# Kernel optimization log

Measured on AMD Instinct MI355X. Metric: run time of the kernel, lower is better.

## Reference

```python
import jax, jax.numpy as jnp
import numpy as np

N = 100000          # total nodes
E = 3200000         # total edges (avg degree 32)
B = 100             # num graphs
NPG = N // B        # nodes per graph (uniform -> to_dense_batch is a reshape)
D_IN, D_H, D_E, N_CLS = 128, 64, 32, 10


def setup_inputs() -> dict:
    key = jax.random.key(0)
    ks = jax.random.split(key, 12)
    x = jax.random.normal(ks[0], (N, D_IN), jnp.float32)
    # edges strictly within each graph: offset by graph block
    epg = E // B
    offs = (jnp.arange(E, dtype=jnp.int32) // epg) * NPG
    src = jax.random.randint(ks[1], (E,), 0, NPG, jnp.int32) + offs
    dst = jax.random.randint(ks[2], (E,), 0, NPG, jnp.int32) + offs
    edge_index = jnp.stack([src, dst])
    batch = jnp.repeat(jnp.arange(B, dtype=jnp.int32), NPG)

    def glorot(k, fi, fo):
        return jax.random.normal(k, (fi, fo), jnp.float32) * (1.0 / np.sqrt(fi))

    return {
        "x": x, "edge_index": edge_index, "batch": batch,
        "W_a1": glorot(ks[3], D_IN, D_H), "b_a1": jnp.zeros((D_H,), jnp.float32),
        "W_a2": glorot(ks[4], D_H, D_E),  "b_a2": jnp.zeros((D_E,), jnp.float32),
        "W_x1": glorot(ks[5], D_IN, D_H), "b_x1": jnp.zeros((D_H,), jnp.float32),
        "W_x2": glorot(ks[6], D_H, D_E),  "b_x2": jnp.zeros((D_E,), jnp.float32),
        "W_lin": glorot(ks[7], D_E * D_E, N_CLS),
        "b_lin": jnp.zeros((N_CLS,), jnp.float32),
    }


def _gcn(x, W, b, src, dst, n):
    """PyG GCNConv(improved=True): sym-norm with self-loop weight 2."""
    h = x @ W                                                   # [n, out]
    deg = jax.ops.segment_sum(jnp.ones_like(dst, h.dtype), dst, n) + 2.0
    dinv = jax.lax.rsqrt(deg)                                   # [n]
    coef = dinv[src] * dinv[dst]                                # [E]
    agg = jax.ops.segment_sum(h[src] * coef[:, None], dst, n)   # gather-scatter
    agg = agg + (2.0 * dinv * dinv)[:, None] * h                # self-loop term
    return agg + b


def _segment_softmax(v, seg, nseg):
    m = jax.ops.segment_max(v, seg, nseg)
    e = jnp.exp(v - m[seg])
    s = jax.ops.segment_sum(e, seg, nseg)
    return e / s[seg]


def reference(x, edge_index, batch, W_a1, b_a1, W_a2, b_a2,
              W_x1, b_x1, W_x2, b_x2, W_lin, b_lin):
    src, dst = edge_index[0], edge_index[1]
    n = x.shape[0]
    a1 = jax.nn.relu(_gcn(x, W_a1, b_a1, src, dst, n))
    a2 = _segment_softmax(_gcn(a1, W_a2, b_a2, src, dst, n), batch, B)
    x1 = jax.nn.relu(_gcn(x, W_x1, b_x1, src, dst, n))
    x2 = jax.nn.relu(_gcn(x1, W_x2, b_x2, src, dst, n))
    # uniform graph sizes -> to_dense_batch is a reshape (no padding needed)
    a_b = a2.reshape(B, NPG, D_E)
    x_b = x2.reshape(B, NPG, D_E)
    prods = jnp.einsum('bne,bnf->bef', a_b, x_b)   # bmm(a^T, x): [B, D_E, D_E]
    flat = prods.reshape(B, D_E * D_E)
    return jax.nn.softmax(flat @ W_lin + b_lin, axis=-1)
```

## Files before the change

kernel.cpp:

```cpp
#include <hip/hip_runtime.h>
#include <hip/hip_bf16.h>
#include <hip/hip_fp16.h>

#define N_NODES 100000
#define N_EDGES 3200000
#define NB      100
#define NPG     1000
#define EPG     32000
#define DIN     128
#define DH      64
#define DE      32
#define NCLS    10
#define SORT_BLOCKS 104


typedef _Float16 h2_t __attribute__((ext_vector_type(2)));
typedef _Float16 h8_t __attribute__((ext_vector_type(8)));
typedef float    f4_t __attribute__((ext_vector_type(4)));

__device__ __forceinline__ float dot2f(unsigned a, unsigned b, float c) {
#if __has_builtin(__builtin_amdgcn_fdot2)
    return __builtin_amdgcn_fdot2(__builtin_bit_cast(h2_t, a),
                                  __builtin_bit_cast(h2_t, b), c, false);
#else
    float d;
    asm("v_dot2_f32_f16 %0, %1, %2, %3" : "=v"(d) : "v"(a), "v"(b), "v"(c));
    return d;
#endif
}

#define DOT8(rA, rB, dv)                                                        \
    acc[0] = dot2f(__builtin_amdgcn_perm(rB.x, rA.x, 0x05040100u), dv, acc[0]); \
    acc[1] = dot2f(__builtin_amdgcn_perm(rB.x, rA.x, 0x07060302u), dv, acc[1]); \
    acc[2] = dot2f(__builtin_amdgcn_perm(rB.y, rA.y, 0x05040100u), dv, acc[2]); \
    acc[3] = dot2f(__builtin_amdgcn_perm(rB.y, rA.y, 0x07060302u), dv, acc[3]); \
    acc[4] = dot2f(__builtin_amdgcn_perm(rB.z, rA.z, 0x05040100u), dv, acc[4]); \
    acc[5] = dot2f(__builtin_amdgcn_perm(rB.z, rA.z, 0x07060302u), dv, acc[5]); \
    acc[6] = dot2f(__builtin_amdgcn_perm(rB.w, rA.w, 0x05040100u), dv, acc[6]); \
    acc[7] = dot2f(__builtin_amdgcn_perm(rB.w, rA.w, 0x07060302u), dv, acc[7]);


union SharedU {
    struct {
        __align__(16) unsigned short buf[EPG];
        int cnt[NPG];
        int pre[NPG];
        int sm[1024];
        unsigned short dh[NPG];
    } so;
    struct {
        __align__(16) unsigned short wt[128 * 128];
    } w1;
};

__global__ __launch_bounds__(1024) void k_sg(const int* __restrict__ src,
                                             const int* __restrict__ dst,
                                             const float* __restrict__ x,
                                             const float* __restrict__ Wa,
                                             const float* __restrict__ Wx,
                                             int* __restrict__ rowptr,
                                             float* __restrict__ dinv,
                                             unsigned int* __restrict__ esrc,
                                             unsigned short* __restrict__ h16) {
    __shared__ SharedU S;
    int t = threadIdx.x;
    if (blockIdx.x < SORT_BLOCKS) {
        int g = (blockIdx.x & 7) + 8 * (blockIdx.x >> 3);
        if (g >= NB) return;
        int ebase = g * EPG, nbase = g * NPG;
        if (t < NPG) S.so.cnt[t] = 0;
        __syncthreads();
        for (int i = t; i < EPG; i += 1024)
            atomicAdd(&S.so.cnt[dst[ebase + i] - nbase], 1);
        __syncthreads();
        int v = (t < NPG) ? S.so.cnt[t] : 0;
        if (t < NPG) {
            float dv = rsqrtf((float)v + 2.0f);
            dinv[nbase + t] = dv;
            S.so.dh[t] = __half_as_ushort(__float2half_rn(dv));
        }
        S.so.sm[t] = v;
        __syncthreads();
        for (int off = 1; off < 1024; off <<= 1) {
            int xx = (t >= off) ? S.so.sm[t - off] : 0;
            __syncthreads();
            S.so.sm[t] += xx;
            __syncthreads();
        }
        if (t < NPG) {
            int ex = S.so.sm[t] - v;
            S.so.pre[t] = ex;
            rowptr[nbase + t] = ebase + ex;
        }
        if (g == NB - 1 && t == 0) rowptr[N_NODES] = N_EDGES;
        __syncthreads();
        for (int i = t; i < EPG; i += 1024) {
            int e = ebase + i;
            int d = dst[e] - nbase;
            int s = src[e] - nbase;
            int pos = atomicAdd(&S.so.pre[d], 1);
            S.so.buf[pos] = (unsigned short)s;
        }
        __syncthreads();
        uint4* gout = (uint4*)(esrc + ebase);
        const ushort4* lbuf = (const ushort4*)S.so.buf;
        for (int i = t; i < EPG / 4; i += 1024) {
            ushort4 s4 = lbuf[i];
            uint4 o;
            o.x = ((unsigned)s4.x * 16) | ((unsigned)S.so.dh[s4.x] << 16);
            o.y = ((unsigned)s4.y * 16) | ((unsigned)S.so.dh[s4.y] << 16);
            o.z = ((unsigned)s4.z * 16) | ((unsigned)S.so.dh[s4.z] << 16);
            o.w = ((unsigned)s4.w * 16) | ((unsigned)S.so.dh[s4.w] << 16);
            gout[i] = o;
        }
    } else {
        int b = blockIdx.x - SORT_BLOCKS;
        int xcd = b & 7, slot = b >> 3;
        int g = xcd + 8 * (slot >> 2);
        int chunk = slot & 3;
        if (g >= NB) return;
        int row0 = g * NPG + chunk * 250;
        for (int j = 0; j < 4; j++) {
            int idx = t + 1024 * j;
            int k = idx >> 5, c = (idx & 31) * 4;
            float4 v;
            if (c < 64) v = *(const float4*)&Wa[k * 64 + c];
            else        v = *(const float4*)&Wx[k * 64 + (c - 64)];
            float vv[4] = {v.x, v.y, v.z, v.w};
            #pragma unroll
            for (int m = 0; m < 4; m++) {
                int cc = c + m;
                int byte = cc * 256 + ((k * 2) ^ ((cc & 7) << 4));
                *(__half*)((char*)S.w1.wt + byte) = __float2half_rn(vv[m]);
            }
        }
        __syncthreads();
        int w = t >> 6, l = t & 63;
        int lr = l & 15, kq = l >> 4;
        int rowA = row0 + w * 16 + lr;
        int rA = rowA < N_NODES ? rowA : N_NODES - 1;
        const float* xr = &x[(size_t)rA * 128];
        h8_t a[4];
        #pragma unroll
        for (int kc = 0; kc < 4; kc++) {
            float4 lo = *(const float4*)&xr[kc * 32 + kq * 8];
            float4 hi = *(const float4*)&xr[kc * 32 + kq * 8 + 4];
            h8_t av;
            av[0] = (_Float16)lo.x; av[1] = (_Float16)lo.y;
            av[2] = (_Float16)lo.z; av[3] = (_Float16)lo.w;
            av[4] = (_Float16)hi.x; av[5] = (_Float16)hi.y;
            av[6] = (_Float16)hi.z; av[7] = (_Float16)hi.w;
            a[kc] = av;
        }
        f4_t acc[8] = {};
        #pragma unroll
        for (int kc = 0; kc < 4; kc++) {
            #pragma unroll
            for (int n = 0; n < 8; n++) {
                int cc = n * 16 + lr;
                int byte = cc * 256 + (((kc * 32 + kq * 8) * 2) ^ ((cc & 7) << 4));
                h8_t bf = *(h8_t*)((char*)S.w1.wt + byte);
                acc[n] = __builtin_amdgcn_mfma_f32_16x16x32_f16(a[kc], bf, acc[n], 0, 0, 0);
            }
        }
        int rowD = row0 + w * 16 + kq * 4;
        #pragma unroll
        for (int n = 0; n < 8; n++) {
            #pragma unroll
            for (int j = 0; j < 4; j++) {
                int r = rowD + j;
                if (r < N_NODES)
                    h16[(size_t)r * 128 + n * 16 + lr] =
                        __half_as_ushort(__float2half_rn(acc[n][j]));
            }
        }
    }
}


__global__ __launch_bounds__(256) void k_agg128(const unsigned short* __restrict__ h16,
                                                const int* __restrict__ rowptr,
                                                const unsigned int* __restrict__ esrc,
                                                const float* __restrict__ dinv,
                                                const float* __restrict__ ba,
                                                const float* __restrict__ bx,
                                                unsigned short* __restrict__ outB16) {
    int xcd = blockIdx.x & 7, slot = blockIdx.x >> 3;
    int gi = slot / 250, chunk = slot - gi * 250;
    int g = xcd + 8 * gi;
    if (g >= NB) return;
    int nl   = chunk * 4 + (threadIdx.x >> 6);
    int wid  = g * NPG + nl;
    int lane = threadIdx.x & 63;
    int sub = lane >> 4;
    int cl  = lane & 15;
    const uint4* hg4 = (const uint4*)(h16 + g * NPG * 128);
    float acc[8] = {};
    union U8 { uint4 u; __half h[8]; };
    int e0 = rowptr[wid], e1 = rowptr[wid + 1];
    int e = e0;
    for (; e + 16 <= e1; e += 16) {
        unsigned pv0 = esrc[e + sub];
        unsigned pv1 = esrc[e + 4 + sub];
        unsigned pv2 = esrc[e + 8 + sub];
        unsigned pv3 = esrc[e + 12 + sub];
        uint4 r0 = hg4[(pv0 & 0xffffu) + cl];
        uint4 r1 = hg4[(pv1 & 0xffffu) + cl];
        uint4 r2 = hg4[(pv2 & 0xffffu) + cl];
        uint4 r3 = hg4[(pv3 & 0xffffu) + cl];
        unsigned dA = __builtin_amdgcn_perm(pv1, pv0, 0x07060302u);
        unsigned dB = __builtin_amdgcn_perm(pv3, pv2, 0x07060302u);
        DOT8(r0, r1, dA);
        DOT8(r2, r3, dB);
    }
    for (; e + 8 <= e1; e += 8) {
        unsigned pv0 = esrc[e + sub];
        unsigned pv1 = esrc[e + 4 + sub];
        uint4 r0 = hg4[(pv0 & 0xffffu) + cl];
        uint4 r1 = hg4[(pv1 & 0xffffu) + cl];
        unsigned dA = __builtin_amdgcn_perm(pv1, pv0, 0x07060302u);
        DOT8(r0, r1, dA);
    }
    for (; e < e1; e += 4) {
        int ee = e + sub;
        unsigned pv; float scale;
        if (ee < e1) { pv = esrc[ee]; scale = 1.0f; }
        else         { pv = esrc[e];  scale = 0.0f; }
        U8 r; r.u = hg4[(pv & 0xffffu) + cl];
        float dv = scale * __half2float(__ushort_as_half((unsigned short)(pv >> 16)));
        #pragma unroll
        for (int k = 0; k < 8; k++)
            acc[k] += dv * __half2float(r.h[k]);
    }
    #pragma unroll
    for (int k = 0; k < 8; k++) {
        acc[k] += __shfl_xor(acc[k], 16);
        acc[k] += __shfl_xor(acc[k], 32);
    }
    if (sub == 0) {
        float di = dinv[wid];
        float sw = 2.0f * di * di;
        U8 hv; hv.u = hg4[nl * 16 + cl];
        int cl8 = cl * 8;
        const float* bb = (cl8 < 64) ? &ba[cl8] : &bx[cl8 - 64];
        union { __half2 h[4]; uint4 q; } pk;
        #pragma unroll
        for (int k = 0; k < 4; k++) {
            float ox = fmaxf(di * acc[2 * k]     + sw * __half2float(hv.h[2 * k])     + bb[2 * k],     0.0f);
            float oy = fmaxf(di * acc[2 * k + 1] + sw * __half2float(hv.h[2 * k + 1]) + bb[2 * k + 1], 0.0f);
            pk.h[k] = __floats2half2_rn(ox, oy);
        }
        *(uint4*)&outB16[wid * 128 + cl8] = pk.q;
    }
}


__global__ __launch_bounds__(256) void k_agg64(const unsigned short* __restrict__ g16,
                                               const int* __restrict__ rowptr,
                                               const unsigned int* __restrict__ esrc,
                                               const float* __restrict__ dinv,
                                               const float* __restrict__ ba2,
                                               const float* __restrict__ bx2,
                                               float* __restrict__ s2) {
    int xcd = blockIdx.x & 7, slot = blockIdx.x >> 3;
    int gi = slot / 250, chunk = slot - gi * 250;
    int g = xcd + 8 * gi;
    if (g >= NB) return;
    int nl   = chunk * 4 + (threadIdx.x >> 6);
    int wid  = g * NPG + nl;
    int lane = threadIdx.x & 63;
    int sub = lane >> 3;
    int cl  = lane & 7;
    const uint4* gg4 = (const uint4*)(g16 + g * NPG * 64);
    float acc[8] = {};
    union U8 { uint4 u; __half h[8]; };
    int e0 = rowptr[wid], e1 = rowptr[wid + 1];
    int e = e0;
    for (; e + 16 <= e1; e += 16) {
        unsigned pv0 = esrc[e + sub];
        unsigned pv1 = esrc[e + 8 + sub];
        uint4 r0 = gg4[((pv0 & 0xffffu) >> 1) + cl];
        uint4 r1 = gg4[((pv1 & 0xffffu) >> 1) + cl];
        unsigned dA = __builtin_amdgcn_perm(pv1, pv0, 0x07060302u);
        DOT8(r0, r1, dA);
    }
    for (; e < e1; e += 8) {
        int ee = e + sub;
        unsigned pv; float scale;
        if (ee < e1) { pv = esrc[ee]; scale = 1.0f; }
        else         { pv = esrc[e];  scale = 0.0f; }
        U8 r; r.u = gg4[((pv & 0xffffu) >> 1) + cl];
        float dv = scale * __half2float(__ushort_as_half((unsigned short)(pv >> 16)));
        #pragma unroll
        for (int k = 0; k < 8; k++)
            acc[k] += dv * __half2float(r.h[k]);
    }
    #pragma unroll
    for (int k = 0; k < 8; k++) {
        acc[k] += __shfl_xor(acc[k], 8);
        acc[k] += __shfl_xor(acc[k], 16);
        acc[k] += __shfl_xor(acc[k], 32);
    }
    if (sub == 0) {
        float di = dinv[wid];
        float sw = 2.0f * di * di;
        U8 hv; hv.u = gg4[nl * 8 + cl];
        int cl8 = cl * 8;
        float o[8];
        #pragma unroll
        for (int k = 0; k < 8; k++)
            o[k] = di * acc[k] + sw * __half2float(hv.h[k]);
        if (cl8 < 32) {
            #pragma unroll
            for (int k = 0; k < 8; k++) o[k] += ba2[cl8 + k];
        } else {
            #pragma unroll
            for (int k = 0; k < 8; k++) o[k] = fmaxf(o[k] + bx2[cl8 - 32 + k], 0.0f);
        }
        *(float4*)&s2[wid * 64 + cl8]     = make_float4(o[0], o[1], o[2], o[3]);
        *(float4*)&s2[wid * 64 + cl8 + 4] = make_float4(o[4], o[5], o[6], o[7]);
    }
}


__global__ __launch_bounds__(256) void k_gemm2(const unsigned short* __restrict__ Bm16,
                                               const float* __restrict__ Wa2,
                                               const float* __restrict__ Wx2,
                                               unsigned short* __restrict__ g16) {
    __shared__ float xs[64][132];
    __shared__ float ws[64][68];
    int xcd = blockIdx.x & 7, slot = blockIdx.x >> 3;
    int g = xcd + 8 * (slot >> 4);
    int chunk = slot & 15;
    if (g >= NB) return;
    int row0 = g * NPG + chunk * 64;
    int t = threadIdx.x;
    for (int i = 0; i < 4; i++) {
        int idx = t + 256 * i;
        int k = idx >> 4, c4 = idx & 15, c = c4 * 4;
        float4 v;
        if (c < 32) v = *(const float4*)&Wa2[k * 32 + c];
        else        v = *(const float4*)&Wx2[k * 32 + (c - 32)];
        *(float4*)&ws[k][c] = v;
    }
    for (int i = 0; i < 4; i++) {
        int idx = t + 256 * i;
        int r = idx >> 4, c8 = idx & 15;
        int rr = row0 + r; if (rr >= N_NODES) rr = N_NODES - 1;
        union { uint4 u; __half2 h[4]; } pk;
        pk.u = *(const uint4*)&Bm16[rr * 128 + c8 * 8];
        float2 f0 = __half22float2(pk.h[0]);
        float2 f1 = __half22float2(pk.h[1]);
        float2 f2 = __half22float2(pk.h[2]);
        float2 f3 = __half22float2(pk.h[3]);
        int cb = c8 * 8;
        *(float4*)&xs[r][cb]     = make_float4(f0.x, f0.y, f1.x, f1.y);
        *(float4*)&xs[r][cb + 4] = make_float4(f2.x, f2.y, f3.x, f3.y);
    }
    __syncthreads();
    int cg = t & 15, rg = t >> 4;
    int koff = (cg < 8) ? 0 : 64;
    float acc[4][4] = {};
    for (int k = 0; k < 64; k++) {
        float4 w = *(float4*)&ws[k][cg * 4];
        float xv[4];
        for (int i = 0; i < 4; i++) xv[i] = xs[rg * 4 + i][koff + k];
        for (int i = 0; i < 4; i++) {
            acc[i][0] += xv[i] * w.x; acc[i][1] += xv[i] * w.y;
            acc[i][2] += xv[i] * w.z; acc[i][3] += xv[i] * w.w;
        }
    }
    for (int i = 0; i < 4; i++) {
        int r = row0 + rg * 4 + i;
        if (r < N_NODES) {
            union { ushort4 u; __half2 h[2]; } pk;
            pk.h[0] = __floats2half2_rn(acc[i][0], acc[i][1]);
            pk.h[1] = __floats2half2_rn(acc[i][2], acc[i][3]);
            *(ushort4*)&g16[r * 64 + cg * 4] = pk.u;
        }
    }
}


__global__ __launch_bounds__(512) void k_smax(const float* __restrict__ s2,
                                              float* __restrict__ gmax,
                                              float* __restrict__ sinv) {
    __shared__ float red[16][32];
    int g = (blockIdx.x & 7) + 8 * (blockIdx.x >> 3);
    if (g >= NB) return;
    int t = threadIdx.x;
    int c = t & 31, sub = t >> 5;
    size_t base = (size_t)g * NPG;
    float m = -1e30f;
    for (int n = sub; n < NPG; n += 16)
        m = fmaxf(m, s2[(base + n) * 64 + c]);
    red[sub][c] = m; __syncthreads();
    if (sub == 0) {
        for (int j = 1; j < 16; j++) m = fmaxf(m, red[j][c]);
        red[0][c] = m;
        gmax[g * 32 + c] = m;
    }
    __syncthreads();
    m = red[0][c];
    __syncthreads();
    float sum = 0.0f;
    for (int n = sub; n < NPG; n += 16)
        sum += __expf(s2[(base + n) * 64 + c] - m);
    red[sub][c] = sum; __syncthreads();
    if (sub == 0) {
        for (int j = 1; j < 16; j++) sum += red[j][c];
        sinv[g * 32 + c] = 1.0f / sum;
    }
}


__global__ __launch_bounds__(256) void k_pool(const float* __restrict__ s2,
                                              const float* __restrict__ gmax,
                                              float* __restrict__ prods) {
    __shared__ float ta[25][32];
    __shared__ float tx[25][32];
    __shared__ float gm[32];
    int xcd = blockIdx.x & 7, slot = blockIdx.x >> 3;
    int g = xcd + 8 * (slot >> 3);
    int ch = slot & 7;
    if (g >= NB) return;
    int t = threadIdx.x;
    if (t < 32) gm[t] = gmax[g * 32 + t];
    int e  = t >> 3;
    int f4 = t & 7;
    float a0 = 0.f, a1 = 0.f, a2 = 0.f, a3 = 0.f;
    int base = g * NPG + ch * 125;
    for (int n0 = 0; n0 < 125; n0 += 25) {
        __syncthreads();
        for (int i = t; i < 25 * 16; i += 256) {
            int r = i >> 4, c4 = i & 15;
            float4 v = *(const float4*)&s2[(size_t)(base + n0 + r) * 64 + c4 * 4];
            if (c4 < 8) {
                int cb = c4 * 4;
                v.x = __expf(v.x - gm[cb + 0]);
                v.y = __expf(v.y - gm[cb + 1]);
                v.z = __expf(v.z - gm[cb + 2]);
                v.w = __expf(v.w - gm[cb + 3]);
                *(float4*)&ta[r][cb] = v;
            } else {
                *(float4*)&tx[r][(c4 - 8) * 4] = v;
            }
        }
        __syncthreads();
        #pragma unroll 5
        for (int n = 0; n < 25; n++) {
            float a   = ta[n][e];
            float4 xv = *(float4*)&tx[n][f4 * 4];
            a0 += a * xv.x; a1 += a * xv.y; a2 += a * xv.z; a3 += a * xv.w;
        }
    }
    *(float4*)&prods[((size_t)(g * 8 + ch)) * 1024 + e * 32 + f4 * 4] =
        make_float4(a0, a1, a2, a3);
}


__global__ __launch_bounds__(256) void k_head(const float* __restrict__ prods,
                                              const float* __restrict__ sinv,
                                              const float* __restrict__ Wlin,
                                              const float* __restrict__ blin,
                                              float* __restrict__ out) {
    __shared__ float red[4][NCLS];
    int g = (blockIdx.x & 7) + 8 * (blockIdx.x >> 3);
    if (g >= NB) return;
    int t = threadIdx.x;
    float p[NCLS];
    for (int c = 0; c < NCLS; c++) p[c] = 0.0f;
    const float* pg = &prods[(size_t)g * 8 * 1024];
    for (int j = 0; j < 4; j++) {
        int k = t * 4 + j;
        int e = k >> 5;
        float v = 0.0f;
        #pragma unroll
        for (int q = 0; q < 8; q++) v += pg[q * 1024 + k];
        v *= sinv[g * 32 + e];
        const float* wrow = &Wlin[k * NCLS];
        for (int c = 0; c < NCLS; c++) p[c] += v * wrow[c];
    }
    for (int off = 32; off > 0; off >>= 1)
        for (int c = 0; c < NCLS; c++) p[c] += __shfl_down(p[c], off, 64);
    int wave = t >> 6, lane = t & 63;
    if (lane == 0)
        for (int c = 0; c < NCLS; c++) red[wave][c] = p[c];
    __syncthreads();
    if (t == 0) {
        float logits[NCLS]; float mx = -1e30f;
        for (int c = 0; c < NCLS; c++) {
            logits[c] = red[0][c] + red[1][c] + red[2][c] + red[3][c] + blin[c];
            mx = fmaxf(mx, logits[c]);
        }
        float s = 0.0f;
        for (int c = 0; c < NCLS; c++) { logits[c] = expf(logits[c] - mx); s += logits[c]; }
        float inv = 1.0f / s;
        for (int c = 0; c < NCLS; c++) out[g * NCLS + c] = logits[c] * inv;
    }
}


extern "C" void kernel_launch(void* const* d_in, const int* in_sizes, int n_in,
                              void* d_out, int out_size, void* d_ws, size_t ws_size,
                              hipStream_t stream) {
    const float* x    = (const float*)d_in[0];
    const int*   ei   = (const int*)d_in[1];
    const float* Wa1  = (const float*)d_in[3];
    const float* ba1  = (const float*)d_in[4];
    const float* Wa2  = (const float*)d_in[5];
    const float* ba2  = (const float*)d_in[6];
    const float* Wx1  = (const float*)d_in[7];
    const float* bx1  = (const float*)d_in[8];
    const float* Wx2  = (const float*)d_in[9];
    const float* bx2  = (const float*)d_in[10];
    const float* Wlin = (const float*)d_in[11];
    const float* blin = (const float*)d_in[12];
    float* out = (float*)d_out;

    char* w = (char*)d_ws;
    auto alloc = [&](size_t bytes) -> void* {
        void* p = (void*)w;
        w += (bytes + 255) & ~(size_t)255;
        return p;
    };
    int*            rowptr = (int*)alloc((N_NODES + 1) * sizeof(int));
    float*          dinv   = (float*)alloc(N_NODES * sizeof(float));
    unsigned int*   esrc   = (unsigned int*)alloc((size_t)N_EDGES * sizeof(unsigned int));
    float*          gmax   = (float*)alloc(NB * DE * sizeof(float));
    float*          sinv   = (float*)alloc(NB * DE * sizeof(float));
    float*          prods  = (float*)alloc((size_t)NB * 8 * 1024 * sizeof(float));
    unsigned short* h16    = (unsigned short*)alloc((size_t)N_NODES * 128 * sizeof(unsigned short));
    unsigned short* b16    = (unsigned short*)alloc((size_t)N_NODES * 128 * sizeof(unsigned short));
    unsigned short* g16    = (unsigned short*)alloc((size_t)N_NODES * 64 * sizeof(unsigned short));
    float*          s2     = (float*)alloc((size_t)N_NODES * 64 * sizeof(float));

    const int* srcp = ei;
    const int* dstp = ei + N_EDGES;

    k_sg<<<SORT_BLOCKS + 8 * 13 * 4, 1024, 0, stream>>>(srcp, dstp, x, Wa1, Wx1,
                                                        rowptr, dinv, esrc, h16);
    k_agg128<<<8 * 13 * 250, 256, 0, stream>>>(h16, rowptr, esrc, dinv, ba1, bx1, b16);
    k_gemm2<<<8 * 13 * 16, 256, 0, stream>>>(b16, Wa2, Wx2, g16);
    k_agg64<<<8 * 13 * 250, 256, 0, stream>>>(g16, rowptr, esrc, dinv, ba2, bx2, s2);
    k_smax<<<8 * 13, 512, 0, stream>>>(s2, gmax, sinv);
    k_pool<<<8 * 13 * 8, 256, 0, stream>>>(s2, gmax, prods);
    k_head<<<8 * 13, 256, 0, stream>>>(prods, sinv, Wlin, blin, out);
}
```

Before: 311.2 us.

## Split per-graph CSR build into parallel count, scan and global-atomic scatter kernels

Replaces the one-block-per-graph CSR sort, which did counting, scan and scatter in shared memory, with three kernels. Each graph's edges are split across 8 sub-blocks for counting, a scan kernel combines the partial counts into rowptr, cursor and fp16 dinv, and the scatter uses global atomics on cursor across 832 blocks. The aim is to spread the sort over far more blocks than 100 graphs allow. The cost is two extra launches, global atomic traffic, and edge order within each row that is no longer deterministic. The W staging into shared memory is also rewritten to pack four halves per store.

```diff
diff --git a/kernel.cpp b/kernel.cpp
--- a/kernel.cpp
+++ b/kernel.cpp
@@ -11,7 +11,7 @@
 #define DH      64
 #define DE      32
 #define NCLS    10
-#define SORT_BLOCKS 104
+#define SCAT_BLOCKS 832
 
 
 typedef _Float16 h2_t __attribute__((ext_vector_type(2)));
@@ -40,98 +40,104 @@
     acc[7] = dot2f(__builtin_amdgcn_perm(rB.w, rA.w, 0x07060302u), dv, acc[7]);
 
 
-union SharedU {
-    struct {
-        __align__(16) unsigned short buf[EPG];
-        int cnt[NPG];
-        int pre[NPG];
-        int sm[1024];
-        unsigned short dh[NPG];
-    } so;
-    struct {
-        __align__(16) unsigned short wt[128 * 128];
-    } w1;
-};
+__global__ __launch_bounds__(256) void k_cnt(const int* __restrict__ dst,
+                                             int* __restrict__ cnt8) {
+    __shared__ int cnt[NPG];
+    int slice = blockIdx.x >> 3;
+    int g = (blockIdx.x & 7) + 8 * (slice % 13);
+    int sub = slice / 13;
+    if (g >= NB) return;
+    int t = threadIdx.x;
+    for (int i = t; i < NPG; i += 256) cnt[i] = 0;
+    __syncthreads();
+    int ebase = g * EPG + sub * 4000, nbase = g * NPG;
+    for (int i = t; i < 4000; i += 256)
+        atomicAdd(&cnt[dst[ebase + i] - nbase], 1);
+    __syncthreads();
+    for (int i = t; i < NPG; i += 256)
+        cnt8[sub * N_NODES + nbase + i] = cnt[i];
+}
+
+
+__global__ __launch_bounds__(1024) void k_scan(const int* __restrict__ cnt8,
+                                               int* __restrict__ rowptr,
+                                               int* __restrict__ cursor,
+                                               float* __restrict__ dinv,
+                                               unsigned short* __restrict__ dh16) {
+    __shared__ int sm[1024];
+    int g = (blockIdx.x & 7) + 8 * (blockIdx.x >> 3);
+    if (g >= NB) return;
+    int t = threadIdx.x;
+    int nbase = g * NPG, ebase = g * EPG;
+    int v = 0;
+    if (t < NPG) {
+        #pragma unroll
+        for (int s8 = 0; s8 < 8; s8++) v += cnt8[s8 * N_NODES + nbase + t];
+        float dv = rsqrtf((float)v + 2.0f);
+        dinv[nbase + t] = dv;
+        dh16[nbase + t] = __half_as_ushort(__float2half_rn(dv));
+    }
+    sm[t] = v;
+    __syncthreads();
+    for (int off = 1; off < 1024; off <<= 1) {
+        int xx = (t >= off) ? sm[t - off] : 0;
+        __syncthreads();
+        sm[t] += xx;
+        __syncthreads();
+    }
+    if (t < NPG) {
+        int ex = ebase + sm[t] - v;
+        rowptr[nbase + t] = ex;
+        cursor[nbase + t] = ex;
+    }
+    if (g == NB - 1 && t == 0) rowptr[N_NODES] = N_EDGES;
+}
+
 
 __global__ __launch_bounds__(1024) void k_sg(const int* __restrict__ src,
                                              const int* __restrict__ dst,
                                              const float* __restrict__ x,
                                              const float* __restrict__ Wa,
                                              const float* __restrict__ Wx,
-                                             int* __restrict__ rowptr,
-                                             float* __restrict__ dinv,
+                                             int* __restrict__ cursor,
+                                             const unsigned short* __restrict__ dh16,
                                              unsigned int* __restrict__ esrc,
                                              unsigned short* __restrict__ h16) {
-    __shared__ SharedU S;
-    int t = threadIdx.x;
-    if (blockIdx.x < SORT_BLOCKS) {
-        int g = (blockIdx.x & 7) + 8 * (blockIdx.x >> 3);
+    __shared__ __align__(16) unsigned short wt[16384];
+    int t = threadIdx.x;
+    if (blockIdx.x < SCAT_BLOCKS) {
+        int slice = blockIdx.x >> 3;
+        int g = (blockIdx.x & 7) + 8 * (slice % 13);
+        int sub = slice / 13;
         if (g >= NB) return;
-        int ebase = g * EPG, nbase = g * NPG;
-        if (t < NPG) S.so.cnt[t] = 0;
-        __syncthreads();
-        for (int i = t; i < EPG; i += 1024)
-            atomicAdd(&S.so.cnt[dst[ebase + i] - nbase], 1);
-        __syncthreads();
-        int v = (t < NPG) ? S.so.cnt[t] : 0;
-        if (t < NPG) {
-            float dv = rsqrtf((float)v + 2.0f);
-            dinv[nbase + t] = dv;
-            S.so.dh[t] = __half_as_ushort(__float2half_rn(dv));
-        }
-        S.so.sm[t] = v;
-        __syncthreads();
-        for (int off = 1; off < 1024; off <<= 1) {
-            int xx = (t >= off) ? S.so.sm[t - off] : 0;
-            __syncthreads();
-            S.so.sm[t] += xx;
-            __syncthreads();
-        }
-        if (t < NPG) {
-            int ex = S.so.sm[t] - v;
-            S.so.pre[t] = ex;
-            rowptr[nbase + t] = ebase + ex;
-        }
-        if (g == NB - 1 && t == 0) rowptr[N_NODES] = N_EDGES;
-        __syncthreads();
-        for (int i = t; i < EPG; i += 1024) {
+        int ebase = g * EPG + sub * 4000, nbase = g * NPG;
+        for (int i = t; i < 4000; i += 1024) {
             int e = ebase + i;
-            int d = dst[e] - nbase;
-            int s = src[e] - nbase;
-            int pos = atomicAdd(&S.so.pre[d], 1);
-            S.so.buf[pos] = (unsigned short)s;
-        }
-        __syncthreads();
-        uint4* gout = (uint4*)(esrc + ebase);
-        const ushort4* lbuf = (const ushort4*)S.so.buf;
-        for (int i = t; i < EPG / 4; i += 1024) {
-            ushort4 s4 = lbuf[i];
-            uint4 o;
-            o.x = ((unsigned)s4.x * 16) | ((unsigned)S.so.dh[s4.x] << 16);
-            o.y = ((unsigned)s4.y * 16) | ((unsigned)S.so.dh[s4.y] << 16);
-            o.z = ((unsigned)s4.z * 16) | ((unsigned)S.so.dh[s4.z] << 16);
-            o.w = ((unsigned)s4.w * 16) | ((unsigned)S.so.dh[s4.w] << 16);
-            gout[i] = o;
+            int d = dst[e];
+            int s = src[e];
+            int pos = atomicAdd(&cursor[d], 1);
+            unsigned rec = ((unsigned)(s - nbase) * 16) | ((unsigned)dh16[s] << 16);
+            esrc[pos] = rec;
         }
     } else {
-        int b = blockIdx.x - SORT_BLOCKS;
-        int xcd = b & 7, slot = b >> 3;
+        int b2 = blockIdx.x - SCAT_BLOCKS;
+        int xcd = b2 & 7, slot = b2 >> 3;
         int g = xcd + 8 * (slot >> 2);
         int chunk = slot & 3;
         if (g >= NB) return;
         int row0 = g * NPG + chunk * 250;
-        for (int j = 0; j < 4; j++) {
-            int idx = t + 1024 * j;
-            int k = idx >> 5, c = (idx & 31) * 4;
-            float4 v;
-            if (c < 64) v = *(const float4*)&Wa[k * 64 + c];
-            else        v = *(const float4*)&Wx[k * 64 + (c - 64)];
-            float vv[4] = {v.x, v.y, v.z, v.w};
+        {
+            int cc = t & 127, kg = t >> 7;
+            const float* Wp = (cc < 64) ? &Wa[cc] : &Wx[cc - 64];
             #pragma unroll
-            for (int m = 0; m < 4; m++) {
-                int cc = c + m;
-                int byte = cc * 256 + ((k * 2) ^ ((cc & 7) << 4));
-                *(__half*)((char*)S.w1.wt + byte) = __float2half_rn(vv[m]);
+            for (int j = 0; j < 4; j++) {
+                int k0 = kg * 16 + j * 4;
+                union { __half h[4]; uint2 u; } pk;
+                #pragma unroll
+                for (int m = 0; m < 4; m++)
+                    pk.h[m] = __float2half_rn(Wp[(k0 + m) * 64]);
+                int byte = cc * 256 + ((2 * k0) ^ ((cc & 7) << 4));
+                *(uint2*)((char*)wt + byte) = pk.u;
             }
         }
         __syncthreads();
@@ -159,7 +165,7 @@
             for (int n = 0; n < 8; n++) {
                 int cc = n * 16 + lr;
                 int byte = cc * 256 + (((kc * 32 + kq * 8) * 2) ^ ((cc & 7) << 4));
-                h8_t bf = *(h8_t*)((char*)S.w1.wt + byte);
+                h8_t bf = *(h8_t*)((char*)wt + byte);
                 acc[n] = __builtin_amdgcn_mfma_f32_16x16x32_f16(a[kc], bf, acc[n], 0, 0, 0);
             }
         }
@@ -525,7 +531,10 @@
         return p;
     };
     int*            rowptr = (int*)alloc((N_NODES + 1) * sizeof(int));
+    int*            cursor = (int*)alloc(N_NODES * sizeof(int));
+    int*            cnt8   = (int*)alloc((size_t)8 * N_NODES * sizeof(int));
     float*          dinv   = (float*)alloc(N_NODES * sizeof(float));
+    unsigned short* dh16   = (unsigned short*)alloc(N_NODES * sizeof(unsigned short));
     unsigned int*   esrc   = (unsigned int*)alloc((size_t)N_EDGES * sizeof(unsigned int));
     float*          gmax   = (float*)alloc(NB * DE * sizeof(float));
     float*          sinv   = (float*)alloc(NB * DE * sizeof(float));
@@ -538,8 +547,10 @@
     const int* srcp = ei;
     const int* dstp = ei + N_EDGES;
 
-    k_sg<<<SORT_BLOCKS + 8 * 13 * 4, 1024, 0, stream>>>(srcp, dstp, x, Wa1, Wx1,
-                                                        rowptr, dinv, esrc, h16);
+    k_cnt<<<SCAT_BLOCKS, 256, 0, stream>>>(dstp, cnt8);
+    k_scan<<<8 * 13, 1024, 0, stream>>>(cnt8, rowptr, cursor, dinv, dh16);
+    k_sg<<<SCAT_BLOCKS + 8 * 13 * 4, 1024, 0, stream>>>(srcp, dstp, x, Wa1, Wx1,
+                                                        cursor, dh16, esrc, h16);
     k_agg128<<<8 * 13 * 250, 256, 0, stream>>>(h16, rowptr, esrc, dinv, ba1, bx1, b16);
     k_gemm2<<<8 * 13 * 16, 256, 0, stream>>>(b16, Wa2, Wx2, g16);
     k_agg64<<<8 * 13 * 250, 256, 0, stream>>>(g16, rowptr, esrc, dinv, ba2, bx2, s2);
```

Result: slower. 388.9 us (+25.0%).
